# Performance work log

Measured on AMD Instinct MI355X. Metric: run time of the kernel, lower is better.

## Reference

```python
import jax, jax.numpy as jnp
import numpy as np

N_NODES = 100000
EMB = 128
E = 800000


def _gcn_conv(x, W, b, src, dst, n_nodes):
    # PyG GCNConv: add self-loops, symmetric normalization D^-1/2 A D^-1/2,
    # linear transform, scatter-add aggregation onto target nodes, + bias.
    ones = jnp.ones(src.shape[0], dtype=x.dtype)
    deg = jax.ops.segment_sum(ones, dst, num_segments=n_nodes) + 1.0  # +1 for self-loop
    dinv = jnp.where(deg > 0, jax.lax.rsqrt(deg), 0.0)
    norm = dinv[src] * dinv[dst]                       # [E]
    h = x @ W                                          # [N, D]
    msg = norm[:, None] * h[src]                       # gather + scale, [E, D]
    out = jax.ops.segment_sum(msg, dst, num_segments=n_nodes)
    out = out + (dinv * dinv)[:, None] * h             # self-loop contribution
    return out + b


def setup_inputs() -> dict:
    key = jax.random.key(0)
    k = jax.random.split(key, 8)
    x = jax.random.normal(k[0], (N_NODES, EMB), dtype=jnp.float32)
    pos_edge_index = jax.random.randint(k[1], (2, E), 0, N_NODES, dtype=jnp.int64)
    neg_edge_index = jax.random.randint(k[2], (2, E), 0, N_NODES, dtype=jnp.int64)
    s = 1.0 / np.sqrt(EMB)
    W0 = jax.random.uniform(k[3], (EMB, EMB), jnp.float32, -s, s)
    b0 = jnp.zeros((EMB,), jnp.float32)
    W1 = jax.random.uniform(k[4], (EMB, EMB), jnp.float32, -s, s)
    b1 = jnp.zeros((EMB,), jnp.float32)
    return {"x": x, "W0": W0, "b0": b0, "W1": W1, "b1": b1,
            "pos_edge_index": pos_edge_index, "neg_edge_index": neg_edge_index}


def reference(x, W0, b0, W1, b1, pos_edge_index, neg_edge_index):
    edge_index = jnp.concatenate([pos_edge_index, neg_edge_index], axis=1)
    src, dst = edge_index[0], edge_index[1]
    z = _gcn_conv(x, W0, b0, src, dst, N_NODES)
    z = _gcn_conv(z, W1, b1, src, dst, N_NODES)
    return z
```

## Files before the change

### kernel.cpp

```cpp
#include <hip/hip_runtime.h>

#define N_NODES 100000
#define EMB 128
#define NE 800000
#define NEDGES (2 * NE)

#define NWIN 256
#define WNODES 391
#define WCAP 8192
#define ACHUNK 2048
#define ABLOCKS ((NEDGES + ACHUNK - 1) / ACHUNK)
#define SEGCAP 7000

typedef __attribute__((ext_vector_type(8))) short bf16x8;
typedef __attribute__((ext_vector_type(4))) float f32x4;
typedef __attribute__((ext_vector_type(2))) float f32x2;


__device__ __forceinline__ unsigned short f2bf(float f) {
    unsigned u = __builtin_bit_cast(unsigned, f);
    u += 0x7FFFu + ((u >> 16) & 1u);
    return (unsigned short)(u >> 16);
}

__device__ __forceinline__ unsigned pk2bf(float lo, float hi) {
    return (unsigned)f2bf(lo) | ((unsigned)f2bf(hi) << 16);
}

__device__ __forceinline__ float bflo(unsigned u) { return __builtin_bit_cast(float, u << 16); }
__device__ __forceinline__ float bfhi(unsigned u) { return __builtin_bit_cast(float, u & 0xFFFF0000u); }

__device__ __forceinline__ f32x2 unpk2(unsigned u) {
    f32x2 r;
    r.x = bflo(u);
    r.y = bfhi(u);
    return r;
}

__global__ void binit_kernel(int* __restrict__ bcur) {
    int w = threadIdx.x;
    if (w < NWIN) bcur[w] = w * WCAP;
}


__global__ __launch_bounds__(256) void binA_kernel(const int* __restrict__ pos,
                                                   const int* __restrict__ neg,
                                                   int* __restrict__ bucket_cursor,
                                                   unsigned* __restrict__ ptmp) {
    __shared__ int lcnt[NWIN];
    __shared__ int lofs[NWIN];
    __shared__ int lcur[NWIN];
    __shared__ int gbase[NWIN];
    __shared__ int stmp[NWIN];
    __shared__ unsigned abuf[ACHUNK];
    __shared__ unsigned char awin[ACHUNK];
    __shared__ unsigned pbuf2[ACHUNK];
    __shared__ unsigned char wbuf2[ACHUNK];

    const int tid  = threadIdx.x;
    const int e0   = blockIdx.x * ACHUNK;
    const int ecnt = (NEDGES - e0 < ACHUNK) ? (NEDGES - e0) : ACHUNK;

    if (tid < NWIN) lcnt[tid] = 0;
    __syncthreads();

    for (int k = tid; k < ecnt; k += 256) {
        int i = e0 + k;
        int s, d;
        if (i < NE) { s = pos[i];      d = pos[NE + i]; }
        else        { s = neg[i - NE]; d = neg[i]; }
        int w = d / WNODES;
        abuf[k] = ((unsigned)(d - w * WNODES) << 17) | (unsigned)s;
        awin[k] = (unsigned char)w;
        atomicAdd(&lcnt[w], 1);
    }
    __syncthreads();

    if (tid < NWIN) stmp[tid] = lcnt[tid];
    __syncthreads();
    for (int off = 1; off < NWIN; off <<= 1) {
        int v = (tid < NWIN && tid >= off) ? stmp[tid - off] : 0;
        __syncthreads();
        if (tid < NWIN) stmp[tid] += v;
        __syncthreads();
    }
    if (tid < NWIN) {
        lofs[tid]  = stmp[tid] - lcnt[tid];
        lcur[tid]  = stmp[tid] - lcnt[tid];
        gbase[tid] = atomicAdd(&bucket_cursor[tid], lcnt[tid]);
    }
    __syncthreads();

    for (int k = tid; k < ecnt; k += 256) {
        int w = awin[k];
        int lp = atomicAdd(&lcur[w], 1);
        pbuf2[lp] = abuf[k];
        wbuf2[lp] = (unsigned char)w;
    }
    __syncthreads();

    for (int k = tid; k < ecnt; k += 256) {
        int w = wbuf2[k];
        ptmp[gbase[w] + (k - lofs[w])] = pbuf2[k];
    }
}


__global__ __launch_bounds__(NWIN) void wscan_kernel(const int* __restrict__ bcur,
                                                     int* __restrict__ wbase) {
    __shared__ int sc[NWIN];
    const int tid = threadIdx.x;
    int t = bcur[tid] - tid * WCAP;
    sc[tid] = t;
    __syncthreads();
    for (int off = 1; off < NWIN; off <<= 1) {
        int v = (tid >= off) ? sc[tid - off] : 0;
        __syncthreads();
        sc[tid] += v;
        __syncthreads();
    }
    wbase[tid] = sc[tid] - t;
}


__global__ __launch_bounds__(1024) void binCB_kernel(const int* __restrict__ bcur,
                                                     const int* __restrict__ wbase,
                                                     const unsigned* __restrict__ ptmp,
                                                     int* __restrict__ rowptr,
                                                     float* __restrict__ dtab,
                                                     unsigned* __restrict__ colidx) {
    __shared__ int cnt[WNODES];
    __shared__ int sc[512];
    __shared__ unsigned stage[WCAP];
    __shared__ unsigned colseg[SEGCAP];

    const int w   = blockIdx.x;
    const int lo  = w * WNODES;
    const int hi  = (lo + WNODES < N_NODES) ? lo + WNODES : N_NODES;
    const int nn  = hi - lo;
    const int tot = bcur[w] - w * WCAP;
    const int tid = threadIdx.x;
    const unsigned* __restrict__ rp = ptmp + (size_t)w * WCAP;

    for (int k = tid; k < nn; k += 1024) cnt[k] = 0;
    __syncthreads();

    for (int k = tid; k < tot; k += 1024) {
        unsigned v = rp[k];
        stage[k] = v;
        atomicAdd(&cnt[v >> 17], 1);
    }
    __syncthreads();

    if (tid < 512) sc[tid] = (tid < nn) ? cnt[tid] : 0;
    __syncthreads();
    for (int off = 1; off < 512; off <<= 1) {
        int v = (tid < 512 && tid >= off) ? sc[tid - off] : 0;
        __syncthreads();
        if (tid < 512) sc[tid] += v;
        __syncthreads();
    }

    const int base = wbase[w];
    int myexc = 0;
    if (tid < nn) {
        myexc = sc[tid] - cnt[tid];
        rowptr[lo + tid]   = base + myexc;
        dtab[lo + tid + 1] = rsqrtf((float)cnt[tid] + 1.0f);
    }
    if (w == 0 && tid == 0) { rowptr[N_NODES] = NEDGES; dtab[0] = 0.0f; }
    __syncthreads();

    if (tid < nn) cnt[tid] = myexc;
    __syncthreads();

    for (int k = tid; k < tot; k += 1024) {
        unsigned v = stage[k];
        int dl = v >> 17;
        unsigned s = (v & 0x1FFFFu) + 1u;
        int lp = atomicAdd(&cnt[dl], 1);
        if (lp < SEGCAP) colseg[lp] = s;
    }
    __syncthreads();

    for (int k = tid; k < tot; k += 1024) colidx[base + k] = colseg[k];
}


#define GROWS 64

template<bool BF16IN>
__global__ __launch_bounds__(256) void gemm_kernel(const void* __restrict__ Xin,
                                                   const float* __restrict__ W,
                                                   unsigned short* __restrict__ Hb) {
    __shared__ unsigned short Wb[128 * 128];

    const int tid  = threadIdx.x;
    const int row0 = blockIdx.x * GROWS;

    for (int i = tid * 4; i < 128 * 128; i += 256 * 4) {
        float4 v = *(const float4*)&W[i];
        int k = i >> 7;
        int c = i & 127;
        int ks = k >> 5;
        int kg = (k >> 3) & 3;
        int j  = k & 7;
        float vv[4] = {v.x, v.y, v.z, v.w};
#pragma unroll
        for (int q = 0; q < 4; ++q) {
            int cc   = c + q;
            int ct   = cc >> 4;
            int lane = (cc & 15) + 16 * kg;
            Wb[((ct * 4 + ks) * 64 + lane) * 8 + j] = f2bf(vv[q]);
        }
    }
    __syncthreads();

    const int wave = tid >> 6;
    const int lane = tid & 63;
    const int r    = lane & 15;
    const int kg   = lane >> 4;

    int row = row0 + wave * 16 + r;
    int rowc = (row < N_NODES) ? row : N_NODES - 1;

    bf16x8 a[4];
    if (BF16IN) {
        const unsigned short* Xb = (const unsigned short*)Xin;
#pragma unroll
        for (int ks = 0; ks < 4; ++ks) {
            a[ks] = *(const bf16x8*)&Xb[(size_t)rowc * EMB + ks * 32 + kg * 8];
        }
    } else {
        const float* Xf = (const float*)Xin;
#pragma unroll
        for (int ks = 0; ks < 4; ++ks) {
            const float4* p = (const float4*)&Xf[(size_t)rowc * EMB + ks * 32 + kg * 8];
            float4 u = p[0];
            float4 v = p[1];
            bf16x8 av;
            av[0] = (short)f2bf(u.x); av[1] = (short)f2bf(u.y);
            av[2] = (short)f2bf(u.z); av[3] = (short)f2bf(u.w);
            av[4] = (short)f2bf(v.x); av[5] = (short)f2bf(v.y);
            av[6] = (short)f2bf(v.z); av[7] = (short)f2bf(v.w);
            a[ks] = av;
        }
    }

    f32x4 acc[8];
#pragma unroll
    for (int ct = 0; ct < 8; ++ct) acc[ct] = (f32x4){0.f, 0.f, 0.f, 0.f};

#pragma unroll
    for (int ct = 0; ct < 8; ++ct) {
#pragma unroll
        for (int ks = 0; ks < 4; ++ks) {
            bf16x8 b = *(bf16x8*)&Wb[((ct * 4 + ks) * 64 + lane) * 8];
            acc[ct] = __builtin_amdgcn_mfma_f32_16x16x32_bf16(a[ks], b, acc[ct], 0, 0, 0);
        }
    }

    const int orow0 = row0 + wave * 16 + (lane >> 4) * 4;
    const int oc    = lane & 15;
#pragma unroll
    for (int reg = 0; reg < 4; ++reg) {
        int orow = orow0 + reg;
        if (orow < N_NODES) {
#pragma unroll
            for (int ct = 0; ct < 8; ++ct) {
                Hb[(size_t)orow * EMB + ct * 16 + oc] = f2bf(acc[ct][reg]);
            }
        }
    }
}


#define AGG_WAVES 4

template<bool STORE_BF16>
__global__ __launch_bounds__(256) void aggregate_kernel(const int* __restrict__ rowptr,
                                                        const unsigned* __restrict__ rec,
                                                        const unsigned* __restrict__ Hb32,
                                                        const float* __restrict__ dtab,
                                                        const float* __restrict__ bias,
                                                        void* __restrict__ outv) {
    const int wave = threadIdx.x >> 6;
    const int lane = threadIdx.x & 63;
    const int node = blockIdx.x * AGG_WAVES + wave;
    if (node >= N_NODES) return;

    const int sub  = lane >> 4;
    const int dl   = lane & 15;
    const unsigned dlo = (unsigned)(dl << 4);

    const int start = rowptr[node];
    const int end   = rowptr[node + 1];

    f32x2 acc2[4];
#pragma unroll
    for (int j = 0; j < 4; ++j) acc2[j] = (f32x2){0.f, 0.f};

    const char* __restrict__ hbase = (const char*)Hb32;

    for (int b = start; b < end; b += 64) {
        int li = b + lane;
        unsigned rl = 0;
        if (li < end) rl = rec[li];
        int nb = end - b; if (nb > 64) nb = 64;
        for (int i = 0; i < nb; i += 16) {
            unsigned rA = __shfl(rl, i + sub,      64);
            unsigned rB = __shfl(rl, i + 4 + sub,  64);
            unsigned rC = __shfl(rl, i + 8 + sub,  64);
            unsigned rD = __shfl(rl, i + 12 + sub, 64);
            float nA = dtab[rA];
            float nB = dtab[rB];
            float nC = dtab[rC];
            float nD = dtab[rD];
            unsigned oA = rA ? (((rA - 1u) << 8) | dlo) : dlo;
            unsigned oB = rB ? (((rB - 1u) << 8) | dlo) : dlo;
            unsigned oC = rC ? (((rC - 1u) << 8) | dlo) : dlo;
            unsigned oD = rD ? (((rD - 1u) << 8) | dlo) : dlo;
            uint4 qA = *(const uint4*)(hbase + oA);
            uint4 qB = *(const uint4*)(hbase + oB);
            uint4 qC = *(const uint4*)(hbase + oC);
            uint4 qD = *(const uint4*)(hbase + oD);
            f32x2 nA2 = (f32x2){nA, nA};
            f32x2 nB2 = (f32x2){nB, nB};
            f32x2 nC2 = (f32x2){nC, nC};
            f32x2 nD2 = (f32x2){nD, nD};
            acc2[0] = __builtin_elementwise_fma(nA2, unpk2(qA.x), acc2[0]);
            acc2[1] = __builtin_elementwise_fma(nA2, unpk2(qA.y), acc2[1]);
            acc2[2] = __builtin_elementwise_fma(nA2, unpk2(qA.z), acc2[2]);
            acc2[3] = __builtin_elementwise_fma(nA2, unpk2(qA.w), acc2[3]);
            acc2[0] = __builtin_elementwise_fma(nB2, unpk2(qB.x), acc2[0]);
            acc2[1] = __builtin_elementwise_fma(nB2, unpk2(qB.y), acc2[1]);
            acc2[2] = __builtin_elementwise_fma(nB2, unpk2(qB.z), acc2[2]);
            acc2[3] = __builtin_elementwise_fma(nB2, unpk2(qB.w), acc2[3]);
            acc2[0] = __builtin_elementwise_fma(nC2, unpk2(qC.x), acc2[0]);
            acc2[1] = __builtin_elementwise_fma(nC2, unpk2(qC.y), acc2[1]);
            acc2[2] = __builtin_elementwise_fma(nC2, unpk2(qC.z), acc2[2]);
            acc2[3] = __builtin_elementwise_fma(nC2, unpk2(qC.w), acc2[3]);
            acc2[0] = __builtin_elementwise_fma(nD2, unpk2(qD.x), acc2[0]);
            acc2[1] = __builtin_elementwise_fma(nD2, unpk2(qD.y), acc2[1]);
            acc2[2] = __builtin_elementwise_fma(nD2, unpk2(qD.z), acc2[2]);
            acc2[3] = __builtin_elementwise_fma(nD2, unpk2(qD.w), acc2[3]);
        }
    }

    float acc[8];
#pragma unroll
    for (int j = 0; j < 4; ++j) { acc[2 * j] = acc2[j].x; acc[2 * j + 1] = acc2[j].y; }

#pragma unroll
    for (int j = 0; j < 8; ++j) {
        acc[j] += __shfl_xor(acc[j], 16, 64);
        acc[j] += __shfl_xor(acc[j], 32, 64);
    }

    if (sub == 0) {
        const float dd = dtab[node + 1];
        const float s2 = dd * dd;
        uint4 q = *(const uint4*)(hbase + (((unsigned)node << 8) | dlo));
        float o[8];
        o[0] = dd * acc[0] + s2 * bflo(q.x);
        o[1] = dd * acc[1] + s2 * bfhi(q.x);
        o[2] = dd * acc[2] + s2 * bflo(q.y);
        o[3] = dd * acc[3] + s2 * bfhi(q.y);
        o[4] = dd * acc[4] + s2 * bflo(q.z);
        o[5] = dd * acc[5] + s2 * bfhi(q.z);
        o[6] = dd * acc[6] + s2 * bflo(q.w);
        o[7] = dd * acc[7] + s2 * bfhi(q.w);

        float4 b0 = *(const float4*)&bias[dl * 8];
        float4 b1 = *(const float4*)&bias[dl * 8 + 4];
        o[0] += b0.x; o[1] += b0.y; o[2] += b0.z; o[3] += b0.w;
        o[4] += b1.x; o[5] += b1.y; o[6] += b1.z; o[7] += b1.w;

        if (STORE_BF16) {
            unsigned short* ob = (unsigned short*)outv;
            uint4 pk;
            pk.x = pk2bf(o[0], o[1]);
            pk.y = pk2bf(o[2], o[3]);
            pk.z = pk2bf(o[4], o[5]);
            pk.w = pk2bf(o[6], o[7]);
            *(uint4*)&ob[(size_t)node * EMB + dl * 8] = pk;
        } else {
            float* of = (float*)outv;
            *(float4*)&of[(size_t)node * EMB + dl * 8]     = make_float4(o[0], o[1], o[2], o[3]);
            *(float4*)&of[(size_t)node * EMB + dl * 8 + 4] = make_float4(o[4], o[5], o[6], o[7]);
        }
    }
}


extern "C" void kernel_launch(void* const* d_in, const int* in_sizes, int n_in,
                              void* d_out, int out_size, void* d_ws, size_t ws_size,
                              hipStream_t stream) {
    const float* x  = (const float*)d_in[0];
    const float* W0 = (const float*)d_in[1];
    const float* b0 = (const float*)d_in[2];
    const float* W1 = (const float*)d_in[3];
    const float* b1 = (const float*)d_in[4];
    const int*   pos = (const int*)d_in[5];
    const int*   neg = (const int*)d_in[6];

    float* ws      = (float*)d_ws;
    float* dtab    = ws;
    unsigned short* hb = (unsigned short*)(ws + 100352);
    int*   rowptr  = (int*)(ws + 6500352);
    int*   bcur    = (int*)(ws + 6600356);
    int*   wbase   = (int*)(ws + 6600612);
    unsigned* ptmp = (unsigned*)(ws + 6600872);
    unsigned* colidx = (unsigned*)(ws + 8698024);
    unsigned short* zb = (unsigned short*)(ws + 10298024);

    binit_kernel<<<1, NWIN, 0, stream>>>(bcur);
    binA_kernel<<<ABLOCKS, 256, 0, stream>>>(pos, neg, bcur, ptmp);
    wscan_kernel<<<1, NWIN, 0, stream>>>(bcur, wbase);
    binCB_kernel<<<NWIN, 1024, 0, stream>>>(bcur, wbase, ptmp, rowptr, dtab, colidx);

    const int agg_grid  = (N_NODES + AGG_WAVES - 1) / AGG_WAVES;
    const int gemm_grid = (N_NODES + GROWS - 1) / GROWS;

    gemm_kernel<false><<<gemm_grid, 256, 0, stream>>>(x, W0, hb);
    aggregate_kernel<true><<<agg_grid, 256, 0, stream>>>(
        rowptr, colidx, (const unsigned*)hb, dtab, b0, zb);

    gemm_kernel<true><<<gemm_grid, 256, 0, stream>>>(zb, W1, hb);
    aggregate_kernel<false><<<agg_grid, 256, 0, stream>>>(
        rowptr, colidx, (const unsigned*)hb, dtab, b1, d_out);
}
```

Baseline: 236.8 us.

## Precompute bf16 MFMA-layout weights once and double GEMM rows per block

Adds a small kernel that converts each weight matrix to bf16 in the MFMA fragment layout once, so each GEMM block copies it into LDS with plain 16-byte loads instead of converting and scattering it. Each block now covers 128 rows (two 16-row tiles per wave), which reuses every LDS B fragment for two MFMAs and halves the number of blocks that reload W. This costs two extra launches, more registers per thread and fewer blocks in flight.

```diff
diff --git a/kernel.cpp b/kernel.cpp
--- a/kernel.cpp
+++ b/kernel.cpp
@@ -187,32 +187,38 @@
 }
 
 
-#define GROWS 64
+__global__ __launch_bounds__(256) void wprep_kernel(const float* __restrict__ W,
+                                                    unsigned* __restrict__ Wbg) {
+    int o2 = blockIdx.x * 256 + threadIdx.x;
+    if (o2 >= 8192) return;
+    int o    = o2 * 2;
+    int ct   = o >> 11;
+    int ks   = (o >> 9) & 3;
+    int lane = (o >> 3) & 63;
+    int j    = o & 7;
+    int k    = ks * 32 + ((lane >> 4) << 3) + j;
+    int c    = (ct << 4) + (lane & 15);
+    float lo = W[k * 128 + c];
+    float hi = W[(k + 1) * 128 + c];
+    Wbg[o2] = pk2bf(lo, hi);
+}
+
+
+#define GROWS 128
 
 template<bool BF16IN>
 __global__ __launch_bounds__(256) void gemm_kernel(const void* __restrict__ Xin,
-                                                   const float* __restrict__ W,
+                                                   const unsigned* __restrict__ Wbg,
                                                    unsigned short* __restrict__ Hb) {
     __shared__ unsigned short Wb[128 * 128];
 
     const int tid  = threadIdx.x;
     const int row0 = blockIdx.x * GROWS;
 
-    for (int i = tid * 4; i < 128 * 128; i += 256 * 4) {
-        float4 v = *(const float4*)&W[i];
-        int k = i >> 7;
-        int c = i & 127;
-        int ks = k >> 5;
-        int kg = (k >> 3) & 3;
-        int j  = k & 7;
-        float vv[4] = {v.x, v.y, v.z, v.w};
-#pragma unroll
-        for (int q = 0; q < 4; ++q) {
-            int cc   = c + q;
-            int ct   = cc >> 4;
-            int lane = (cc & 15) + 16 * kg;
-            Wb[((ct * 4 + ks) * 64 + lane) * 8 + j] = f2bf(vv[q]);
-        }
+#pragma unroll
+    for (int i = 0; i < 8; ++i) {
+        int idx = tid + i * 256;
+        ((uint4*)Wb)[idx] = ((const uint4*)Wbg)[idx];
     }
     __syncthreads();
 
@@ -221,55 +227,73 @@
     const int r    = lane & 15;
     const int kg   = lane >> 4;
 
-    int row = row0 + wave * 16 + r;
-    int rowc = (row < N_NODES) ? row : N_NODES - 1;
-
-    bf16x8 a[4];
+    int rowA = row0 + wave * 16 + r;
+    int rowB = rowA + 64;
+    int rowAc = (rowA < N_NODES) ? rowA : N_NODES - 1;
+    int rowBc = (rowB < N_NODES) ? rowB : N_NODES - 1;
+
+    bf16x8 a0[4], a1[4];
     if (BF16IN) {
         const unsigned short* Xb = (const unsigned short*)Xin;
 #pragma unroll
         for (int ks = 0; ks < 4; ++ks) {
-            a[ks] = *(const bf16x8*)&Xb[(size_t)rowc * EMB + ks * 32 + kg * 8];
+            a0[ks] = *(const bf16x8*)&Xb[(size_t)rowAc * EMB + ks * 32 + kg * 8];
+            a1[ks] = *(const bf16x8*)&Xb[(size_t)rowBc * EMB + ks * 32 + kg * 8];
         }
     } else {
         const float* Xf = (const float*)Xin;
 #pragma unroll
         for (int ks = 0; ks < 4; ++ks) {
-            const float4* p = (const float4*)&Xf[(size_t)rowc * EMB + ks * 32 + kg * 8];
-            float4 u = p[0];
-            float4 v = p[1];
-            bf16x8 av;
-            av[0] = (short)f2bf(u.x); av[1] = (short)f2bf(u.y);
-            av[2] = (short)f2bf(u.z); av[3] = (short)f2bf(u.w);
-            av[4] = (short)f2bf(v.x); av[5] = (short)f2bf(v.y);
-            av[6] = (short)f2bf(v.z); av[7] = (short)f2bf(v.w);
-            a[ks] = av;
-        }
-    }
-
-    f32x4 acc[8];
-#pragma unroll
-    for (int ct = 0; ct < 8; ++ct) acc[ct] = (f32x4){0.f, 0.f, 0.f, 0.f};
+            const float4* pA = (const float4*)&Xf[(size_t)rowAc * EMB + ks * 32 + kg * 8];
+            const float4* pB = (const float4*)&Xf[(size_t)rowBc * EMB + ks * 32 + kg * 8];
+            float4 uA = pA[0], vA = pA[1];
+            float4 uB = pB[0], vB = pB[1];
+            bf16x8 avA, avB;
+            avA[0] = (short)f2bf(uA.x); avA[1] = (short)f2bf(uA.y);
+            avA[2] = (short)f2bf(uA.z); avA[3] = (short)f2bf(uA.w);
+            avA[4] = (short)f2bf(vA.x); avA[5] = (short)f2bf(vA.y);
+            avA[6] = (short)f2bf(vA.z); avA[7] = (short)f2bf(vA.w);
+            avB[0] = (short)f2bf(uB.x); avB[1] = (short)f2bf(uB.y);
+            avB[2] = (short)f2bf(uB.z); avB[3] = (short)f2bf(uB.w);
+            avB[4] = (short)f2bf(vB.x); avB[5] = (short)f2bf(vB.y);
+            avB[6] = (short)f2bf(vB.z); avB[7] = (short)f2bf(vB.w);
+            a0[ks] = avA;
+            a1[ks] = avB;
+        }
+    }
+
+    f32x4 acc0[8], acc1[8];
+#pragma unroll
+    for (int ct = 0; ct < 8; ++ct) {
+        acc0[ct] = (f32x4){0.f, 0.f, 0.f, 0.f};
+        acc1[ct] = (f32x4){0.f, 0.f, 0.f, 0.f};
+    }
 
 #pragma unroll
     for (int ct = 0; ct < 8; ++ct) {
 #pragma unroll
         for (int ks = 0; ks < 4; ++ks) {
             bf16x8 b = *(bf16x8*)&Wb[((ct * 4 + ks) * 64 + lane) * 8];
-            acc[ct] = __builtin_amdgcn_mfma_f32_16x16x32_bf16(a[ks], b, acc[ct], 0, 0, 0);
-        }
-    }
-
-    const int orow0 = row0 + wave * 16 + (lane >> 4) * 4;
+            acc0[ct] = __builtin_amdgcn_mfma_f32_16x16x32_bf16(a0[ks], b, acc0[ct], 0, 0, 0);
+            acc1[ct] = __builtin_amdgcn_mfma_f32_16x16x32_bf16(a1[ks], b, acc1[ct], 0, 0, 0);
+        }
+    }
+
     const int oc    = lane & 15;
+    const int obase = row0 + wave * 16 + (lane >> 4) * 4;
 #pragma unroll
     for (int reg = 0; reg < 4; ++reg) {
-        int orow = orow0 + reg;
-        if (orow < N_NODES) {
-#pragma unroll
-            for (int ct = 0; ct < 8; ++ct) {
-                Hb[(size_t)orow * EMB + ct * 16 + oc] = f2bf(acc[ct][reg]);
-            }
+        int orowA = obase + reg;
+        int orowB = orowA + 64;
+        if (orowA < N_NODES) {
+#pragma unroll
+            for (int ct = 0; ct < 8; ++ct)
+                Hb[(size_t)orowA * EMB + ct * 16 + oc] = f2bf(acc0[ct][reg]);
+        }
+        if (orowB < N_NODES) {
+#pragma unroll
+            for (int ct = 0; ct < 8; ++ct)
+                Hb[(size_t)orowB * EMB + ct * 16 + oc] = f2bf(acc1[ct][reg]);
         }
     }
 }
@@ -413,20 +437,25 @@
     unsigned* ptmp = (unsigned*)(ws + 6600872);
     unsigned* colidx = (unsigned*)(ws + 8698024);
     unsigned short* zb = (unsigned short*)(ws + 10298024);
+    unsigned* wbg0 = (unsigned*)(ws + 16698024);
+    unsigned* wbg1 = (unsigned*)(ws + 16706216);
 
     binit_kernel<<<1, NWIN, 0, stream>>>(bcur);
     binA_kernel<<<ABLOCKS, 256, 0, stream>>>(pos, neg, bcur, ptmp);
     wscan_kernel<<<1, NWIN, 0, stream>>>(bcur, wbase);
     binCB_kernel<<<NWIN, 1024, 0, stream>>>(bcur, wbase, ptmp, rowptr, dtab, colidx);
 
+    wprep_kernel<<<32, 256, 0, stream>>>(W0, wbg0);
+    wprep_kernel<<<32, 256, 0, stream>>>(W1, wbg1);
+
     const int agg_grid  = (N_NODES + AGG_WAVES - 1) / AGG_WAVES;
     const int gemm_grid = (N_NODES + GROWS - 1) / GROWS;
 
-    gemm_kernel<false><<<gemm_grid, 256, 0, stream>>>(x, W0, hb);
+    gemm_kernel<false><<<gemm_grid, 256, 0, stream>>>(x, wbg0, hb);
     aggregate_kernel<true><<<agg_grid, 256, 0, stream>>>(
         rowptr, colidx, (const unsigned*)hb, dtab, b0, zb);
 
-    gemm_kernel<true><<<gemm_grid, 256, 0, stream>>>(zb, W1, hb);
+    gemm_kernel<true><<<gemm_grid, 256, 0, stream>>>(zb, wbg1, hb);
     aggregate_kernel<false><<<agg_grid, 256, 0, stream>>>(
         rowptr, colidx, (const unsigned*)hb, dtab, b1, d_out);
 }
```

After: 206.6 us. 12.8% less time.
